# Optimization experiments

Measured on AMD Instinct MI355X. Metric: run time of the kernel, lower is better.

Reference implementation:

```python
import jax, jax.numpy as jnp
import numpy as np

H = 16
D_MODEL = 1024
D_K = D_MODEL // H
L = 4096


def setup_inputs() -> dict:
    key = jax.random.key(0)
    ks = jax.random.split(key, 11)
    s = 1.0 / np.sqrt(D_MODEL)
    inp = {
        "query": jax.random.normal(ks[0], (L, D_MODEL), dtype=jnp.float32),
        "key": jax.random.normal(ks[1], (L, D_MODEL), dtype=jnp.float32),
        "value": jax.random.normal(ks[2], (L, D_MODEL), dtype=jnp.float32),
        "Wq": jax.random.uniform(ks[3], (D_MODEL, D_MODEL), jnp.float32, -s, s),
        "Wk": jax.random.uniform(ks[4], (D_MODEL, D_MODEL), jnp.float32, -s, s),
        "Wv": jax.random.uniform(ks[5], (D_MODEL, D_MODEL), jnp.float32, -s, s),
        "Wo": jax.random.uniform(ks[6], (D_MODEL, D_MODEL), jnp.float32, -s, s),
        "bq": jax.random.uniform(ks[7], (D_MODEL,), jnp.float32, -s, s),
        "bk": jax.random.uniform(ks[8], (D_MODEL,), jnp.float32, -s, s),
        "bv": jax.random.uniform(ks[9], (D_MODEL,), jnp.float32, -s, s),
        "bo": jax.random.uniform(ks[10], (D_MODEL,), jnp.float32, -s, s),
    }
    return inp


def reference(query, key, value, Wq, Wk, Wv, Wo, bq, bk, bv, bo):
    # projections: torch Linear computes x @ W.T + b
    def proj(x, W, b):
        # [L, d_model] -> [h, L, d_k]
        y = x @ W.T + b
        return y.reshape(L, H, D_K).transpose(1, 0, 2)

    q = proj(query, Wq, bq)   # [h, L, d_k]
    k = proj(key, Wk, bk)
    v = proj(value, Wv, bv)

    scores = jnp.einsum("hqd,hkd->hqk", q, k) / jnp.sqrt(jnp.float32(D_K))  # [h, L, L]
    p = jax.nn.softmax(scores, axis=-1)
    x = jnp.einsum("hqk,hkd->hqd", p, v)         # [h, L, d_k]
    x = x.transpose(1, 0, 2).reshape(L, H * D_K)  # [L, d_model]
    return x @ Wo.T + bo
```

## Files before the change

kernel.cpp:

```cpp
#include <hip/hip_runtime.h>

#define L_SEQ 4096
#define DM 1024
#define NH 16
#define DK 64

typedef short s16x8 __attribute__((ext_vector_type(8)));
typedef float f32x4 __attribute__((ext_vector_type(4)));
typedef float f32x8 __attribute__((ext_vector_type(8)));
typedef float f32x16 __attribute__((ext_vector_type(16)));
typedef unsigned u32x2 __attribute__((ext_vector_type(2)));
typedef unsigned short u16t;
typedef unsigned int u32t;

typedef __attribute__((address_space(1))) unsigned int as1_u32;
typedef __attribute__((address_space(3))) unsigned int as3_u32;

#define GLOAD_LDS16(gsrc, ldst) \
  __builtin_amdgcn_global_load_lds((as1_u32*)(gsrc), (as3_u32*)(ldst), 16, 0, 0)

__device__ __forceinline__ u16t f2bf(float f) {
  union { float f; unsigned u; } v; v.f = f;
  unsigned u = v.u;
  u += 0x7fffu + ((u >> 16) & 1u);
  return (u16t)(u >> 16);
}

__device__ __forceinline__ float fexp2(float x) {
  float r;
  asm("v_exp_f32 %0, %1" : "=v"(r) : "v"(x));
  return r;
}

__device__ __forceinline__ float bflo(u32t u) {
  union { u32t u; float f; } v; v.u = u << 16; return v.f;
}
__device__ __forceinline__ float bfhi(u32t u) {
  union { u32t u; float f; } v; v.u = u & 0xffff0000u; return v.f;
}

struct CvtArgs { const float* s[7]; u16t* d[7]; };

__global__ __launch_bounds__(256) void cvt_all(CvtArgs a) {
  int g = blockIdx.x * 256 + threadIdx.x;
  int seg, off;
  if (g < 1572864) { seg = g >> 19;               off = g & 524287; }
  else             { int t = g - 1572864; seg = 3 + (t >> 17); off = t & 131071; }
  const float* src = a.s[seg] + (size_t)off * 8;
  u16t* dst = a.d[seg] + (size_t)off * 8;
  float4 x = *(const float4*)(src);
  float4 y = *(const float4*)(src + 4);
  uint4 o;
  o.x = (u32t)f2bf(x.x) | ((u32t)f2bf(x.y) << 16);
  o.y = (u32t)f2bf(x.z) | ((u32t)f2bf(x.w) << 16);
  o.z = (u32t)f2bf(y.x) | ((u32t)f2bf(y.y) << 16);
  o.w = (u32t)f2bf(y.z) | ((u32t)f2bf(y.w) << 16);
  *(uint4*)dst = o;
}

struct QkvArgs {
  const u16t* A[3]; const u16t* Bm[3]; const float* bias[3]; u16t* C[3];
  float scale0;
};

__global__ __launch_bounds__(256)
void gemm_qkv(QkvArgs ga) {
  __shared__ unsigned char lds[2][2][8192];
  const int flat = blockIdx.x;
  const int bid = (flat & 7) * 96 + (flat >> 3);
  const int z = bid >> 8;
  const int b = bid & 255;
  const int bc = (z == 2) ? (b & 31) : (b & 7);
  const int br = (z == 2) ? (b >> 5) : (b >> 3);
  const int N  = (z == 2) ? L_SEQ : DM;
  const float osc = (z == 0) ? ga.scale0 : 1.0f;
  const bool rowb = (z == 2);
  const u16t* A = ga.A[z];
  const u16t* Bm = ga.Bm[z];
  const float* bias = ga.bias[z];
  u16t* C = ga.C[z];
  const int K = DM;

  const int tid = threadIdx.x;
  const int lane = tid & 63;
  const int wv = tid >> 6;
  const int wr = wv >> 1, wc = wv & 1;
  const int l15 = lane & 15, l4 = lane >> 4;

  const int r_st = tid >> 2;
  const int c_st = (tid & 3) ^ ((r_st >> 1) & 3);
  const u16t* a0 = A + (size_t)(br * 128 + r_st) * K + c_st * 8;
  const u16t* a1 = a0 + (size_t)64 * K;
  const u16t* b0 = Bm + (size_t)(bc * 128 + r_st) * K + c_st * 8;
  const u16t* b1 = b0 + (size_t)64 * K;
  const int woff = wv * 1024;

  f32x4 acc[4][4] = {};

  auto stage = [&](int buf, int k0) {
    GLOAD_LDS16(a0 + k0, &lds[buf][0][woff]);
    GLOAD_LDS16(a1 + k0, &lds[buf][0][4096 + woff]);
    GLOAD_LDS16(b0 + k0, &lds[buf][1][woff]);
    GLOAD_LDS16(b1 + k0, &lds[buf][1][4096 + woff]);
  };

  const int nt = K >> 5;
  stage(0, 0);
  int buf = 0;
  for (int t = 0; t < nt; ++t) {
    __syncthreads();
    if (t + 1 < nt) stage(buf ^ 1, (t + 1) * 32);
    s16x8 af[4], bfr[4];
    #pragma unroll
    for (int m = 0; m < 4; ++m) {
      int r = wr * 64 + m * 16 + l15;
      int sl = l4 ^ ((r >> 1) & 3);
      af[m] = *(const s16x8*)&lds[buf][0][r * 64 + (sl << 4)];
    }
    #pragma unroll
    for (int n = 0; n < 4; ++n) {
      int r = wc * 64 + n * 16 + l15;
      int sl = l4 ^ ((r >> 1) & 3);
      bfr[n] = *(const s16x8*)&lds[buf][1][r * 64 + (sl << 4)];
    }
    #pragma unroll
    for (int m = 0; m < 4; ++m)
      #pragma unroll
      for (int n = 0; n < 4; ++n)
        acc[m][n] = __builtin_amdgcn_mfma_f32_16x16x32_bf16(af[m], bfr[n], acc[m][n], 0, 0, 0);
    buf ^= 1;
  }

  #pragma unroll
  for (int m = 0; m < 4; ++m) {
    #pragma unroll
    for (int n = 0; n < 4; ++n) {
      #pragma unroll
      for (int i = 0; i < 4; ++i) {
        int row = br * 128 + wr * 64 + m * 16 + l4 * 4 + i;
        int col = bc * 128 + wc * 64 + n * 16 + l15;
        float v = (acc[m][n][i] + (rowb ? bias[row] : bias[col])) * osc;
        C[(size_t)row * N + col] = f2bf(v);
      }
    }
  }
}

__global__ __launch_bounds__(256)
void gemm_out(const u16t* __restrict__ A, const u16t* __restrict__ B,
              const float* __restrict__ bias, float* __restrict__ C,
              int M, int N, int K) {
  __shared__ unsigned char lds[2][12288];
  const int tid = threadIdx.x;
  const int lane = tid & 63;
  const int wv = tid >> 6;
  const int wr = wv >> 1, wc = wv & 1;
  const int l15 = lane & 15, l4 = lane >> 4;
  const int flat = blockIdx.x + (blockIdx.y << 4);
  const int nsw = (flat & 7) * 64 + (flat >> 3);
  const int bc = nsw & 15, br = nsw >> 4;

  const int r_st = tid >> 2;
  const int c_st = (tid & 3) ^ ((r_st >> 1) & 3);
  const u16t* a0 = A + (size_t)(br * 128 + r_st) * K + c_st * 8;
  const u16t* a1 = a0 + (size_t)64 * K;
  const u16t* b0 = B + (size_t)(bc * 64 + r_st) * K + c_st * 8;
  const int woff = wv * 1024;

  f32x4 acc[4][2] = {};

  auto stage = [&](int buf, int k0) {
    GLOAD_LDS16(a0 + k0, &lds[buf][woff]);
    GLOAD_LDS16(a1 + k0, &lds[buf][4096 + woff]);
    GLOAD_LDS16(b0 + k0, &lds[buf][8192 + woff]);
  };

  const int nt = K >> 5;
  stage(0, 0);
  int buf = 0;
  for (int t = 0; t < nt; ++t) {
    __syncthreads();
    if (t + 1 < nt) stage(buf ^ 1, (t + 1) * 32);
    s16x8 af[4], bfr[2];
    #pragma unroll
    for (int m = 0; m < 4; ++m) {
      int r = wr * 64 + m * 16 + l15;
      int sl = l4 ^ ((r >> 1) & 3);
      af[m] = *(const s16x8*)&lds[buf][r * 64 + (sl << 4)];
    }
    #pragma unroll
    for (int n = 0; n < 2; ++n) {
      int r = wc * 32 + n * 16 + l15;
      int sl = l4 ^ ((r >> 1) & 3);
      bfr[n] = *(const s16x8*)&lds[buf][8192 + r * 64 + (sl << 4)];
    }
    #pragma unroll
    for (int m = 0; m < 4; ++m)
      #pragma unroll
      for (int n = 0; n < 2; ++n)
        acc[m][n] = __builtin_amdgcn_mfma_f32_16x16x32_bf16(af[m], bfr[n], acc[m][n], 0, 0, 0);
    buf ^= 1;
  }

  #pragma unroll
  for (int m = 0; m < 4; ++m) {
    #pragma unroll
    for (int n = 0; n < 2; ++n) {
      #pragma unroll
      for (int i = 0; i < 4; ++i) {
        int row = br * 128 + wr * 64 + m * 16 + l4 * 4 + i;
        int col = bc * 64 + wc * 32 + n * 16 + l15;
        C[(size_t)row * N + col] = acc[m][n][i] + bias[col];
      }
    }
  }
}

#define PKBF(dst, a, b) \
  asm("v_cvt_pk_bf16_f32 %0, %1, %2" : "=v"(dst) : "v"(a), "v"(b))

#define MAKE_FRAG(S, B, FR) { \
    u32t w0, w1, w2, w3; \
    PKBF(w0, S[B + 0], S[B + 1]); PKBF(w1, S[B + 2], S[B + 3]); \
    PKBF(w2, S[B + 4], S[B + 5]); PKBF(w3, S[B + 6], S[B + 7]); \
    u32x2 r02 = __builtin_amdgcn_permlane32_swap(w0, w2, false, false); \
    u32x2 r13 = __builtin_amdgcn_permlane32_swap(w1, w3, false, false); \
    union { u32t u[4]; s16x8 v; } uu; \
    uu.u[0] = r02[0]; uu.u[1] = r13[0]; uu.u[2] = r02[1]; uu.u[3] = r13[1]; \
    FR = uu.v; }

__global__ __launch_bounds__(512, 4)
void attn_fused(const u16t* __restrict__ Qp, const u16t* __restrict__ Kp,
                const u16t* __restrict__ VpT, u16t* __restrict__ Op,
                float* __restrict__ Ml) {
  __shared__ unsigned char sStage[3][16384];

  const int tid = threadIdx.x;
  const int lane = tid & 63;
  const int w = tid >> 6;
  const int l31 = lane & 31;
  const int hi = lane >> 5;
  const int flat = blockIdx.x;
  const int nsw = (flat & 7) * 96 + (flat >> 3);
  const int qt = nsw & 15;
  const int h = (nsw >> 4) & 15;
  const int z = nsw >> 8;
  const int nt = (z == 2) ? 22 : 21;
  const int kvbase = z * 1344;
  const int qrow = qt * 256 + w * 32 + l31;
  u16t* Opz = Op + (size_t)z * (L_SEQ * DM);
  float* Mlz = Ml + z * (NH * L_SEQ);

  s16x8 qf[4];
  {
    const u16t* qsrc = Qp + (size_t)qrow * DM + h * DK + hi * 8;
    #pragma unroll
    for (int c = 0; c < 4; ++c) qf[c] = *(const s16x8*)(qsrc + c * 16);
  }

  f32x16 acc0 = {}, acc1 = {};
  float lrow = 0.f;

  const u16t* kptr = Kp + (size_t)(kvbase + lane) * DM + h * DK + w * 8;
  const u16t* vptr = VpT + (size_t)(h * DK + lane) * L_SEQ + kvbase + w * 8;
  const int woffK = w * 1024;

  auto stage = [&](int buf) {
    GLOAD_LDS16(kptr, &sStage[buf][woffK]);
    GLOAD_LDS16(vptr, &sStage[buf][8192 + woffK]);
    kptr += 64 * DM;
    vptr += 64;
  };

  const int rdoff = (hi << 10) + (l31 << 4);

  auto compute = [&](const unsigned char* sb) {
    f32x16 st0 = {}, st1 = {};
    __builtin_amdgcn_s_setprio(1);
    #pragma unroll
    for (int c = 0; c < 4; ++c) {
      s16x8 kf0 = *(const s16x8*)(sb + c * 2048);
      s16x8 kf1 = *(const s16x8*)(sb + c * 2048 + 512);
      st0 = __builtin_amdgcn_mfma_f32_32x32x16_bf16(kf0, qf[c], st0, 0, 0, 0);
      st1 = __builtin_amdgcn_mfma_f32_32x32x16_bf16(kf1, qf[c], st1, 0, 0, 0);
    }
    __builtin_amdgcn_s_setprio(0);

    #pragma unroll
    for (int r = 0; r < 16; ++r) {
      st0[r] = fexp2(st0[r]);
      st1[r] = fexp2(st1[r]);
    }
    f32x16 sv = st0 + st1;
    f32x8 s8v = __builtin_shufflevector(sv, sv, 0, 1, 2, 3, 4, 5, 6, 7) +
                __builtin_shufflevector(sv, sv, 8, 9, 10, 11, 12, 13, 14, 15);
    f32x4 s4v = __builtin_shufflevector(s8v, s8v, 0, 1, 2, 3) +
                __builtin_shufflevector(s8v, s8v, 4, 5, 6, 7);
    lrow += (s4v[0] + s4v[1]) + (s4v[2] + s4v[3]);

    __builtin_amdgcn_s_setprio(1);
    #pragma unroll
    for (int cc = 0; cc < 4; ++cc) {
      s16x8 pfr;
      if (cc == 0)      MAKE_FRAG(st0, 0, pfr)
      else if (cc == 1) MAKE_FRAG(st0, 8, pfr)
      else if (cc == 2) MAKE_FRAG(st1, 0, pfr)
      else              MAKE_FRAG(st1, 8, pfr)
      s16x8 vf0 = *(const s16x8*)(sb + 8192 + cc * 2048);
      s16x8 vf1 = *(const s16x8*)(sb + 8192 + cc * 2048 + 512);
      acc0 = __builtin_amdgcn_mfma_f32_32x32x16_bf16(vf0, pfr, acc0, 0, 0, 0);
      acc1 = __builtin_amdgcn_mfma_f32_32x32x16_bf16(vf1, pfr, acc1, 0, 0, 0);
    }
    __builtin_amdgcn_s_setprio(0);
  };

  stage(0);
  stage(1);
  int cur = 0, nst = 2;
  #pragma unroll 1
  for (int t = 0; t < nt - 2; ++t) {
    asm volatile("s_waitcnt vmcnt(2)" ::: "memory");
    __builtin_amdgcn_s_barrier();
    __builtin_amdgcn_sched_barrier(0);
    stage(nst);
    nst = (nst == 2) ? 0 : nst + 1;
    compute(sStage[cur] + rdoff);
    cur = (cur == 2) ? 0 : cur + 1;
  }
  asm volatile("s_waitcnt vmcnt(2)" ::: "memory");
  __builtin_amdgcn_s_barrier();
  __builtin_amdgcn_sched_barrier(0);
  compute(sStage[cur] + rdoff);
  cur = (cur == 2) ? 0 : cur + 1;
  asm volatile("s_waitcnt vmcnt(0)" ::: "memory");
  __builtin_amdgcn_s_barrier();
  __builtin_amdgcn_sched_barrier(0);
  compute(sStage[cur] + rdoff);

  lrow += __shfl_xor(lrow, 32);
  u16t* orow = Opz + (size_t)qrow * DM + h * DK;
  #pragma unroll
  for (int rq = 0; rq < 4; ++rq) {
    union { u16t h4[4]; uint2 v; } p0, p1;
    #pragma unroll
    for (int i = 0; i < 4; ++i) {
      p0.h4[i] = f2bf(acc0[4 * rq + i]);
      p1.h4[i] = f2bf(acc1[4 * rq + i]);
    }
    int d0 = 8 * rq + 4 * hi;
    *(uint2*)(orow + d0)      = p0.v;
    *(uint2*)(orow + 32 + d0) = p1.v;
  }
  if (hi == 0) Mlz[h * L_SEQ + qrow] = lrow;
}

__global__ __launch_bounds__(256)
void attn_combine(const u16t* __restrict__ Op, const float* __restrict__ Ml,
                  u16t* __restrict__ AO) {
  int g = blockIdx.x * 256 + threadIdx.x;
  int qh = g >> 2;
  int d0 = (g & 3) * 16;
  int q = qh >> 4, h = qh & 15;
  size_t off = (size_t)q * DM + h * DK + d0;
  const size_t OSTR = (size_t)L_SEQ * DM;

  int mi = h * L_SEQ + q;
  float inv = 1.0f / (Ml[mi] + Ml[NH * L_SEQ + mi] + Ml[2 * NH * L_SEQ + mi]);

  uint4 a[2], b[2], c[2], o[2];
  a[0] = *(const uint4*)(Op + off);             a[1] = *(const uint4*)(Op + off + 8);
  b[0] = *(const uint4*)(Op + OSTR + off);      b[1] = *(const uint4*)(Op + OSTR + off + 8);
  c[0] = *(const uint4*)(Op + 2 * OSTR + off);  c[1] = *(const uint4*)(Op + 2 * OSTR + off + 8);
  #pragma unroll
  for (int k = 0; k < 2; ++k) {
    u32t* au = (u32t*)&a[k]; u32t* bu = (u32t*)&b[k];
    u32t* cu = (u32t*)&c[k]; u32t* ou = (u32t*)&o[k];
    #pragma unroll
    for (int j = 0; j < 4; ++j) {
      float lo = (bflo(au[j]) + bflo(bu[j]) + bflo(cu[j])) * inv;
      float hf = (bfhi(au[j]) + bfhi(bu[j]) + bfhi(cu[j])) * inv;
      ou[j] = (u32t)f2bf(lo) | ((u32t)f2bf(hf) << 16);
    }
  }
  *(uint4*)(AO + off)     = o[0];
  *(uint4*)(AO + off + 8) = o[1];
}

extern "C" void kernel_launch(void* const* d_in, const int* in_sizes, int n_in,
                              void* d_out, int out_size, void* d_ws, size_t ws_size,
                              hipStream_t stream) {
  const float* query = (const float*)d_in[0];
  const float* key_  = (const float*)d_in[1];
  const float* value = (const float*)d_in[2];
  const float* Wq = (const float*)d_in[3];
  const float* Wk = (const float*)d_in[4];
  const float* Wv = (const float*)d_in[5];
  const float* Wo = (const float*)d_in[6];
  const float* bq = (const float*)d_in[7];
  const float* bk = (const float*)d_in[8];
  const float* bv = (const float*)d_in[9];
  const float* bo = (const float*)d_in[10];

  char* ws = (char*)d_ws;
  const size_t MB = 1u << 20;
  u16t* qb  = (u16t*)(ws + 0 * MB);
  u16t* kb  = (u16t*)(ws + 8 * MB);
  u16t* vb  = (u16t*)(ws + 16 * MB);
  u16t* wqb = (u16t*)(ws + 24 * MB);
  u16t* wkb = (u16t*)(ws + 26 * MB);
  u16t* wvb = (u16t*)(ws + 28 * MB);
  u16t* wob = (u16t*)(ws + 30 * MB);
  u16t* Qp  = (u16t*)(ws + 32 * MB);
  u16t* Kp  = (u16t*)(ws + 40 * MB);
  u16t* VpT = (u16t*)(ws + 48 * MB);
  u16t* AO  = (u16t*)(ws + 56 * MB);

  u16t* Op  = (u16t*)(ws + 0 * MB);
  float* Ml = (float*)(ws + 24 * MB);

  const float QSCALE = 0.125f * 1.4426950408889634f;

  CvtArgs ca;
  ca.s[0] = query; ca.s[1] = key_; ca.s[2] = value;
  ca.s[3] = Wq; ca.s[4] = Wk; ca.s[5] = Wv; ca.s[6] = Wo;
  ca.d[0] = qb; ca.d[1] = kb; ca.d[2] = vb;
  ca.d[3] = wqb; ca.d[4] = wkb; ca.d[5] = wvb; ca.d[6] = wob;
  cvt_all<<<dim3(8192), dim3(256), 0, stream>>>(ca);

  QkvArgs ga;
  ga.A[0] = qb;  ga.Bm[0] = wqb; ga.bias[0] = bq; ga.C[0] = Qp;
  ga.A[1] = kb;  ga.Bm[1] = wkb; ga.bias[1] = bk; ga.C[1] = Kp;
  ga.A[2] = wvb; ga.Bm[2] = vb;  ga.bias[2] = bv; ga.C[2] = VpT;
  ga.scale0 = QSCALE;
  gemm_qkv<<<dim3(768), dim3(256), 0, stream>>>(ga);

  attn_fused<<<dim3(768), dim3(512), 0, stream>>>(Qp, Kp, VpT, Op, Ml);

  attn_combine<<<dim3(1024), dim3(256), 0, stream>>>(Op, Ml, AO);

  gemm_out<<<dim3(DM / 64, L_SEQ / 128), dim3(256), 0, stream>>>(
      AO, wob, bo, (float*)d_out, L_SEQ, DM, DM);
}
```

Baseline: 155.9 us.

## Split KV into two halves, unroll stage ring, drop permlane swap via V column permutation

The attention kernel now splits the key sequence into two halves instead of three uneven chunks, launching 512 blocks, and the combine kernel merges two partials. The stage ring loop is unrolled by three with fixed buffer indices so the modulo-index bookkeeping disappears. The permlane32 swap in P-fragment construction is removed; to compensate, the V-transpose projection output permutes columns within each 16-group so the MFMA operand layouts still match. Fewer blocks (512 on the device's CUs) may change occupancy and load balance, but reduce partial-output traffic.

```diff
diff --git a/kernel.cpp b/kernel.cpp
--- a/kernel.cpp
+++ b/kernel.cpp
@@ -9,7 +9,6 @@
 typedef float f32x4 __attribute__((ext_vector_type(4)));
 typedef float f32x8 __attribute__((ext_vector_type(8)));
 typedef float f32x16 __attribute__((ext_vector_type(16)));
-typedef unsigned u32x2 __attribute__((ext_vector_type(2)));
 typedef unsigned short u16t;
 typedef unsigned int u32t;
 
@@ -131,6 +130,8 @@
     buf ^= 1;
   }
 
+  const int l15p = rowb ? ((l15 & 3) | ((l15 & 4) << 1) | ((l15 & 8) >> 1)) : l15;
+
   #pragma unroll
   for (int m = 0; m < 4; ++m) {
     #pragma unroll
@@ -138,7 +139,7 @@
       #pragma unroll
       for (int i = 0; i < 4; ++i) {
         int row = br * 128 + wr * 64 + m * 16 + l4 * 4 + i;
-        int col = bc * 128 + wc * 64 + n * 16 + l15;
+        int col = bc * 128 + wc * 64 + n * 16 + l15p;
         float v = (acc[m][n][i] + (rowb ? bias[row] : bias[col])) * osc;
         C[(size_t)row * N + col] = f2bf(v);
       }
@@ -220,13 +221,11 @@
   asm("v_cvt_pk_bf16_f32 %0, %1, %2" : "=v"(dst) : "v"(a), "v"(b))
 
 #define MAKE_FRAG(S, B, FR) { \
-    u32t w0, w1, w2, w3; \
-    PKBF(w0, S[B + 0], S[B + 1]); PKBF(w1, S[B + 2], S[B + 3]); \
-    PKBF(w2, S[B + 4], S[B + 5]); PKBF(w3, S[B + 6], S[B + 7]); \
-    u32x2 r02 = __builtin_amdgcn_permlane32_swap(w0, w2, false, false); \
-    u32x2 r13 = __builtin_amdgcn_permlane32_swap(w1, w3, false, false); \
     union { u32t u[4]; s16x8 v; } uu; \
-    uu.u[0] = r02[0]; uu.u[1] = r13[0]; uu.u[2] = r02[1]; uu.u[3] = r13[1]; \
+    PKBF(uu.u[0], S[B + 0], S[B + 1]); \
+    PKBF(uu.u[1], S[B + 2], S[B + 3]); \
+    PKBF(uu.u[2], S[B + 4], S[B + 5]); \
+    PKBF(uu.u[3], S[B + 6], S[B + 7]); \
     FR = uu.v; }
 
 __global__ __launch_bounds__(512, 4)
@@ -241,12 +240,11 @@
   const int l31 = lane & 31;
   const int hi = lane >> 5;
   const int flat = blockIdx.x;
-  const int nsw = (flat & 7) * 96 + (flat >> 3);
+  const int nsw = (flat & 7) * 64 + (flat >> 3);
   const int qt = nsw & 15;
   const int h = (nsw >> 4) & 15;
   const int z = nsw >> 8;
-  const int nt = (z == 2) ? 22 : 21;
-  const int kvbase = z * 1344;
+  const int kvbase = z * (L_SEQ / 2);
   const int qrow = qt * 256 + w * 32 + l31;
   u16t* Opz = Op + (size_t)z * (L_SEQ * DM);
   float* Mlz = Ml + z * (NH * L_SEQ);
@@ -314,28 +312,30 @@
     __builtin_amdgcn_s_setprio(0);
   };
 
-  stage(0);
-  stage(1);
-  int cur = 0, nst = 2;
-  #pragma unroll 1
-  for (int t = 0; t < nt - 2; ++t) {
+  auto phase = [&](int bc, int bs) {
     asm volatile("s_waitcnt vmcnt(2)" ::: "memory");
     __builtin_amdgcn_s_barrier();
     __builtin_amdgcn_sched_barrier(0);
-    stage(nst);
-    nst = (nst == 2) ? 0 : nst + 1;
-    compute(sStage[cur] + rdoff);
-    cur = (cur == 2) ? 0 : cur + 1;
+    stage(bs);
+    compute(sStage[bc] + rdoff);
+  };
+
+  stage(0);
+  stage(1);
+  #pragma unroll 1
+  for (int c = 0; c < 10; ++c) {
+    phase(0, 2);
+    phase(1, 0);
+    phase(2, 1);
   }
   asm volatile("s_waitcnt vmcnt(2)" ::: "memory");
   __builtin_amdgcn_s_barrier();
   __builtin_amdgcn_sched_barrier(0);
-  compute(sStage[cur] + rdoff);
-  cur = (cur == 2) ? 0 : cur + 1;
+  compute(sStage[0] + rdoff);
   asm volatile("s_waitcnt vmcnt(0)" ::: "memory");
   __builtin_amdgcn_s_barrier();
   __builtin_amdgcn_sched_barrier(0);
-  compute(sStage[cur] + rdoff);
+  compute(sStage[1] + rdoff);
 
   lrow += __shfl_xor(lrow, 32);
   u16t* orow = Opz + (size_t)qrow * DM + h * DK;
@@ -365,20 +365,18 @@
   const size_t OSTR = (size_t)L_SEQ * DM;
 
   int mi = h * L_SEQ + q;
-  float inv = 1.0f / (Ml[mi] + Ml[NH * L_SEQ + mi] + Ml[2 * NH * L_SEQ + mi]);
-
-  uint4 a[2], b[2], c[2], o[2];
-  a[0] = *(const uint4*)(Op + off);             a[1] = *(const uint4*)(Op + off + 8);
-  b[0] = *(const uint4*)(Op + OSTR + off);      b[1] = *(const uint4*)(Op + OSTR + off + 8);
-  c[0] = *(const uint4*)(Op + 2 * OSTR + off);  c[1] = *(const uint4*)(Op + 2 * OSTR + off + 8);
+  float inv = 1.0f / (Ml[mi] + Ml[NH * L_SEQ + mi]);
+
+  uint4 a[2], b[2], o[2];
+  a[0] = *(const uint4*)(Op + off);         a[1] = *(const uint4*)(Op + off + 8);
+  b[0] = *(const uint4*)(Op + OSTR + off);  b[1] = *(const uint4*)(Op + OSTR + off + 8);
   #pragma unroll
   for (int k = 0; k < 2; ++k) {
-    u32t* au = (u32t*)&a[k]; u32t* bu = (u32t*)&b[k];
-    u32t* cu = (u32t*)&c[k]; u32t* ou = (u32t*)&o[k];
+    u32t* au = (u32t*)&a[k]; u32t* bu = (u32t*)&b[k]; u32t* ou = (u32t*)&o[k];
     #pragma unroll
     for (int j = 0; j < 4; ++j) {
-      float lo = (bflo(au[j]) + bflo(bu[j]) + bflo(cu[j])) * inv;
-      float hf = (bfhi(au[j]) + bfhi(bu[j]) + bfhi(cu[j])) * inv;
+      float lo = (bflo(au[j]) + bflo(bu[j])) * inv;
+      float hf = (bfhi(au[j]) + bfhi(bu[j])) * inv;
       ou[j] = (u32t)f2bf(lo) | ((u32t)f2bf(hf) << 16);
     }
   }
@@ -416,7 +414,7 @@
   u16t* AO  = (u16t*)(ws + 56 * MB);
 
   u16t* Op  = (u16t*)(ws + 0 * MB);
-  float* Ml = (float*)(ws + 24 * MB);
+  float* Ml = (float*)(ws + 16 * MB);
 
   const float QSCALE = 0.125f * 1.4426950408889634f;
 
@@ -434,7 +432,7 @@
   ga.scale0 = QSCALE;
   gemm_qkv<<<dim3(768), dim3(256), 0, stream>>>(ga);
 
-  attn_fused<<<dim3(768), dim3(512), 0, stream>>>(Qp, Kp, VpT, Op, Ml);
+  attn_fused<<<dim3(512), dim3(512), 0, stream>>>(Qp, Kp, VpT, Op, Ml);
 
   attn_combine<<<dim3(1024), dim3(256), 0, stream>>>(Op, Ml, AO);
 
```

Result: faster. 149.0 us (-4.4%).
